# Performance work log

Measured on AMD Instinct MI355X. Metric: run time of the kernel, lower is better.

The kernel has to match this reference:

```python
import jax, jax.numpy as jnp
import numpy as np
import math

EMBED_DIM = 2048
NUM_HEADS = 16
DEPTH = 12
HEAD_DIM = EMBED_DIM // NUM_HEADS // 2  # 64
LAMBDA_INIT = 0.8 - 0.6 * math.exp(-0.3 * DEPTH)


def setup_inputs() -> dict:
    key = jax.random.key(0)
    ks = jax.random.split(key, 9)
    B, T, E = 2, 2048, EMBED_DIM
    s = 1.0 / math.sqrt(E)
    return {
        "query": jax.random.normal(ks[0], (B, T, E), jnp.float32),
        "Wq": jax.random.normal(ks[1], (E, E), jnp.float32) * s,
        "Wk": jax.random.normal(ks[2], (E, E), jnp.float32) * s,
        "Wv": jax.random.normal(ks[3], (E, E), jnp.float32) * s,
        "Wo": jax.random.normal(ks[4], (E, E), jnp.float32) * s,
        "lambda_q1": jax.random.normal(ks[5], (HEAD_DIM,), jnp.float32) * 0.1,
        "lambda_k1": jax.random.normal(ks[6], (HEAD_DIM,), jnp.float32) * 0.1,
        "lambda_q2": jax.random.normal(ks[7], (HEAD_DIM,), jnp.float32) * 0.1,
        "lambda_k2": jax.random.normal(ks[8], (HEAD_DIM,), jnp.float32) * 0.1,
        "subln_weight": jnp.ones((2 * HEAD_DIM,), jnp.float32),
    }


def _diff_attn(query, Wq, Wk, Wv, Wo, lq1, lk1, lq2, lk2, g):
    B, T, E = query.shape
    H, D = NUM_HEADS, HEAD_DIM
    S = T  # self-attention: key = value = query
    scaling = D ** -0.5

    # projections (nn.Linear: x @ W.T)
    q = (query @ Wq.T).reshape(B, T, 2 * H, D).transpose(0, 2, 1, 3)  # [B,2H,T,D]
    k = (query @ Wk.T).reshape(B, S, 2 * H, D).transpose(0, 2, 1, 3)  # [B,2H,S,D]
    v = (query @ Wv.T).reshape(B, S, H, 2 * D).transpose(0, 2, 1, 3)  # [B,H,S,2D]

    q = q * scaling
    attn = jnp.einsum("bhtd,bhsd->bhts", q, k)  # [B,2H,T,S]
    attn = jnp.nan_to_num(attn)
    # default causal mask (offset = S - T = 0)
    causal = jnp.triu(jnp.full((T, S), -jnp.inf, attn.dtype), k=1)
    attn = jax.nn.softmax(attn + causal, axis=-1)

    lam1 = jnp.exp(jnp.sum(lq1 * lk1))
    lam2 = jnp.exp(jnp.sum(lq2 * lk2))
    lam = lam1 - lam2 + LAMBDA_INIT

    attn = attn.reshape(B, H, 2, T, S)
    attn = attn[:, :, 0] - lam * attn[:, :, 1]  # differential combine [B,H,T,S]

    out = jnp.einsum("bhts,bhsd->bhtd", attn, v)  # [B,H,T,2D]
    # RMSNorm over last dim (2D), eps=1e-5, elementwise affine g
    rms = jax.lax.rsqrt(jnp.mean(out * out, axis=-1, keepdims=True) + 1e-5)
    out = out * rms * g
    out = out * (1.0 - LAMBDA_INIT)
    out = out.transpose(0, 2, 1, 3).reshape(B, T, H * 2 * D)
    return out @ Wo.T


def reference(query, Wq, Wk, Wv, Wo, lambda_q1, lambda_k1, lambda_q2, lambda_k2, subln_weight):
    return _diff_attn(query, Wq, Wk, Wv, Wo, lambda_q1, lambda_k1, lambda_q2, lambda_k2, subln_weight)
```

## Files before the change

### kernel.cpp

```cpp
#include <hip/hip_runtime.h>


#define B_SZ   2
#define T_LEN  2048
#define E_DIM  2048
#define M_ROWS 4096
#define NH     16
#define HH     32
#define HD     64
#define VD     128
#define NQT    16
#define QKLD   4096

#define LAMBDA_INIT_F 0.7836057665316239f
#define ONE_MINUS_LI  0.2163942334683761f

typedef __attribute__((ext_vector_type(4))) float          f32x4;
typedef __attribute__((ext_vector_type(8))) short          s16x8;
typedef __attribute__((ext_vector_type(4))) unsigned short u16x4;
typedef __attribute__((ext_vector_type(8))) __bf16         bf16x8;

typedef const __attribute__((address_space(1))) unsigned int* gas_t;
typedef __attribute__((address_space(3))) unsigned int*       las_t;
__device__ __forceinline__ void gl_lds16(const void* g, void* l) {
  __builtin_amdgcn_global_load_lds((gas_t)g, (las_t)l, 16, 0, 0);
}

__device__ __forceinline__ float bf2f(unsigned short h) {
  union { unsigned u; float f; } v; v.u = ((unsigned)h) << 16; return v.f;
}
__device__ __forceinline__ unsigned short f2bf(float f) {
  union { float f; unsigned u; } v; v.f = f;
  return (unsigned short)((v.u + 0x7fffu + ((v.u >> 16) & 1u)) >> 16);
}
__device__ __forceinline__ unsigned fbits(float f) {
  union { float f; unsigned u; } v; v.f = f; return v.u;
}
__device__ __forceinline__ float bits2f(unsigned u) {
  union { unsigned u; float f; } v; v.u = u; return v.f;
}

__global__ __launch_bounds__(256) void cast_bf16(const float* __restrict__ in,
                                                 unsigned short* __restrict__ out,
                                                 int n4, float scale) {
  int i = blockIdx.x * 256 + threadIdx.x;
  const int stride = gridDim.x * 256;
  for (; i < n4; i += stride) {
    f32x4 v = ((const f32x4*)in)[i];
    u16x4 o;
    o[0] = f2bf(v[0] * scale); o[1] = f2bf(v[1] * scale);
    o[2] = f2bf(v[2] * scale); o[3] = f2bf(v[3] * scale);
    ((u16x4*)out)[i] = o;
  }
}

template <int OUT_F32>
__global__ __launch_bounds__(512, 2) void gemm8(const unsigned short* __restrict__ A,
                                                const unsigned short* __restrict__ Bm,
                                                void* __restrict__ Cout,
                                                int M, int N, int K, float alpha,
                                                int gx) {
  __shared__ unsigned short AS[2][2][128 * 64];
  __shared__ unsigned short BS[2][2][128 * 64];
  const int tid = threadIdx.x, lane = tid & 63, wave = tid >> 6;
  const int wm = wave >> 2, wn = wave & 3;
  const int lr = lane & 15, g = lane >> 4;
  const int nwg = gridDim.x;
  const int cpx = nwg >> 3;
  const int bid = blockIdx.x;
  const int swz = (bid & 7) * cpx + (bid >> 3);
  const int bx = swz % gx, by = swz / gx;
  const int m0 = bx * 256, n0 = by * 256;

  f32x4 acc[8][4] = {};
  const int NT = K >> 6;

  auto stageA = [&](int t, int h) {
#pragma unroll
    for (int l = 0; l < 2; ++l) {
      const int ci = l * 512 + tid;
      const int row = ci >> 3;
      const int cs = (ci & 7) ^ (row & 7);
      gl_lds16(A + (size_t)(m0 + h * 128 + row) * K + t * 64 + cs * 8,
               &AS[t & 1][h][(l * 512 + wave * 64) * 8]);
    }
  };
  auto stageB = [&](int t, int h) {
#pragma unroll
    for (int l = 0; l < 2; ++l) {
      const int ci = l * 512 + tid;
      const int row = ci >> 3;
      const int cs = (ci & 7) ^ (row & 7);
      gl_lds16(Bm + (size_t)(n0 + h * 128 + row) * K + t * 64 + cs * 8,
               &BS[t & 1][h][(l * 512 + wave * 64) * 8]);
    }
  };

  stageA(0, 0); stageB(0, 0); stageA(0, 1); stageB(0, 1);
  asm volatile("s_waitcnt vmcnt(4)" ::: "memory");
  __builtin_amdgcn_sched_barrier(0);
  __builtin_amdgcn_s_barrier();

  for (int t = 0; t < NT; ++t) {
    const int cur = t & 1;
    const bool pf = (t + 1 < NT);
#pragma unroll
    for (int p = 0; p < 4; ++p) {
      const int mh = p & 1;
      const int nh = p >> 1;
      bf16x8 af[4][2], bfr[2][2];
#pragma unroll
      for (int mf = 0; mf < 4; ++mf) {
        const int r = wm * 64 + mf * 16 + lr;
#pragma unroll
        for (int kc = 0; kc < 2; ++kc)
          af[mf][kc] = *(const bf16x8*)(&AS[cur][mh][r * 64 + (((kc * 4 + g) ^ (r & 7)) * 8)]);
      }
#pragma unroll
      for (int nf = 0; nf < 2; ++nf) {
        const int r = wn * 32 + nf * 16 + lr;
#pragma unroll
        for (int kc = 0; kc < 2; ++kc)
          bfr[nf][kc] = *(const bf16x8*)(&BS[cur][nh][r * 64 + (((kc * 4 + g) ^ (r & 7)) * 8)]);
      }
      if (pf) {
        if (p == 0)      stageA(t + 1, 0);
        else if (p == 1) stageB(t + 1, 0);
        else if (p == 2) stageA(t + 1, 1);
        else             stageB(t + 1, 1);
      }
      __builtin_amdgcn_s_barrier();
      __builtin_amdgcn_s_setprio(1);
#pragma unroll
      for (int mf = 0; mf < 4; ++mf)
#pragma unroll
        for (int nf = 0; nf < 2; ++nf)
#pragma unroll
          for (int kc = 0; kc < 2; ++kc)
            acc[mh * 4 + mf][nh * 2 + nf] =
                __builtin_amdgcn_mfma_f32_16x16x32_bf16(af[mf][kc], bfr[nf][kc],
                                                        acc[mh * 4 + mf][nh * 2 + nf],
                                                        0, 0, 0);
      __builtin_amdgcn_s_setprio(0);
      if (p == 2) asm volatile("s_waitcnt vmcnt(6)" ::: "memory");
      else        asm volatile("s_waitcnt vmcnt(4)" ::: "memory");
      __builtin_amdgcn_sched_barrier(0);
      __builtin_amdgcn_s_barrier();
    }
  }

#pragma unroll
  for (int mh = 0; mh < 2; ++mh)
#pragma unroll
    for (int mf = 0; mf < 4; ++mf)
#pragma unroll
      for (int nh = 0; nh < 2; ++nh)
#pragma unroll
        for (int nf = 0; nf < 2; ++nf) {
          const int rowb = m0 + mh * 128 + wm * 64 + mf * 16 + g * 4;
          const int col  = n0 + nh * 128 + wn * 32 + nf * 16 + lr;
#pragma unroll
          for (int r = 0; r < 4; ++r) {
            const float v = acc[mh * 4 + mf][nh * 2 + nf][r] * alpha;
            const size_t idx = (size_t)(rowb + r) * N + col;
            if (OUT_F32) ((float*)Cout)[idx] = v;
            else         ((unsigned short*)Cout)[idx] = f2bf(v);
          }
        }
}

__device__ __forceinline__ void stage_kv(const unsigned short* __restrict__ Kbase,
                                         const unsigned short* __restrict__ Vbase,
                                         int s0, unsigned short* KsBuf,
                                         unsigned short* VtBuf, int tid, int wave) {
#pragma unroll
  for (int j = 0; j < 2; ++j) {
    const int ci = tid + j * 256;
    const int s = ci >> 3;
    const int cs = (ci & 7) ^ (s & 7);
    gl_lds16(Kbase + (size_t)(s0 + s) * QKLD + cs * 8, KsBuf + (wave * 64 + j * 256) * 8);
  }
#pragma unroll
  for (int cc = 0; cc < 4; ++cc) {
    const int ci = tid + cc * 256;
    const int d = ci >> 3;
    const int cs = (ci & 7) ^ (d & 7);
    gl_lds16(Vbase + (size_t)d * M_ROWS + s0 + cs * 8, VtBuf + (wave * 64 + cc * 256) * 8);
  }
}

__global__ __launch_bounds__(256, 2) void flash_attn_mfma(
    const unsigned short* __restrict__ QK,
    const unsigned short* __restrict__ VT,
    float* __restrict__ Ohalf) {
  const int pr = blockIdx.x;
  const int hh = blockIdx.y;
  const int b  = blockIdx.z;
  const int tid = threadIdx.x, lane = tid & 63, wave = tid >> 6;
  const int g = lane >> 4, lr = lane & 15;
  const int h = hh >> 1;
  const size_t bT = (size_t)b * T_LEN;

  __shared__ unsigned short Ks[2][64 * 64];
  __shared__ unsigned short Vt[2][128 * 64];
  __shared__ unsigned short Pl[128 * 64];

  const unsigned short* Kbase = QK + bT * QKLD + E_DIM + hh * HD;
  const unsigned short* Vbase = VT + (size_t)(h * VD) * M_ROWS + b * T_LEN;

#pragma unroll 1
  for (int half = 0; half < 2; ++half) {
    const int qt = half ? (NQT - 1 - pr) : pr;
    const int qbase = qt * 128;
    const int rw0 = qbase + wave * 32;

    bf16x8 qf[2][2];
#pragma unroll
    for (int mi = 0; mi < 2; ++mi)
#pragma unroll
      for (int kc = 0; kc < 2; ++kc) {
        const int row = qbase + wave * 32 + mi * 16 + lr;
        qf[mi][kc] = *(const bf16x8*)(QK + (bT + row) * QKLD + hh * HD + kc * 32 + g * 8);
      }

    f32x4 Oa[2][8];
#pragma unroll
    for (int mi = 0; mi < 2; ++mi)
#pragma unroll
      for (int dv = 0; dv < 8; ++dv) Oa[mi][dv] = (f32x4){0.f, 0.f, 0.f, 0.f};
    float m_run[2][4], l_part[2][4];
#pragma unroll
    for (int mi = 0; mi < 2; ++mi)
#pragma unroll
      for (int r = 0; r < 4; ++r) { m_run[mi][r] = -1e30f; l_part[mi][r] = 0.f; }

    const int nsteps = 2 * qt + 2;
    __syncthreads();
    stage_kv(Kbase, Vbase, 0, Ks[0], Vt[0], tid, wave);
    int cb = 0;

    for (int ti = 0; ti < nsteps; ++ti) {
      const int s0 = ti * 64;
      __syncthreads();
      if (ti + 1 < nsteps)
        stage_kv(Kbase, Vbase, s0 + 64, Ks[cb ^ 1], Vt[cb ^ 1], tid, wave);

      if (s0 <= rw0 + 31) {
        const unsigned short* ks = Ks[cb];
        const unsigned short* vt = Vt[cb];
        bf16x8 kb[4][2];
#pragma unroll
        for (int nj = 0; nj < 4; ++nj)
#pragma unroll
          for (int kc = 0; kc < 2; ++kc) {
            const int srow = nj * 16 + lr;
            kb[nj][kc] = *(const bf16x8*)(&ks[srow * 64 + (((kc * 4 + g) ^ (srow & 7)) * 8)]);
          }
        f32x4 Sa[2][4];
#pragma unroll
        for (int mi = 0; mi < 2; ++mi)
#pragma unroll
          for (int nj = 0; nj < 4; ++nj) {
            f32x4 acc = (f32x4){0.f, 0.f, 0.f, 0.f};
#pragma unroll
            for (int kc = 0; kc < 2; ++kc)
              acc = __builtin_amdgcn_mfma_f32_16x16x32_bf16(qf[mi][kc], kb[nj][kc], acc, 0, 0, 0);
            Sa[mi][nj] = acc;
          }

        const bool needmask = (s0 + 63) > rw0;
        float mx[2][4];
        bool anew = false;
#pragma unroll
        for (int mi = 0; mi < 2; ++mi)
#pragma unroll
          for (int r = 0; r < 4; ++r) {
            const int rowq = rw0 + mi * 16 + g * 4 + r;
            float m0v = -1e30f;
#pragma unroll
            for (int nj = 0; nj < 4; ++nj) {
              float v = Sa[mi][nj][r];
              if (needmask && (s0 + nj * 16 + lr > rowq)) v = -1e30f;
              Sa[mi][nj][r] = v;
              m0v = fmaxf(m0v, v);
            }
            m0v = fmaxf(m0v, __shfl_xor(m0v, 1));
            m0v = fmaxf(m0v, __shfl_xor(m0v, 2));
            m0v = fmaxf(m0v, __shfl_xor(m0v, 4));
            m0v = fmaxf(m0v, __shfl_xor(m0v, 8));
            mx[mi][r] = m0v;
            anew |= (m0v > m_run[mi][r] + 8.0f);
          }

        if (__any(anew)) {
#pragma unroll
          for (int mi = 0; mi < 2; ++mi)
#pragma unroll
            for (int r = 0; r < 4; ++r) {
              const float mn = fmaxf(m_run[mi][r], mx[mi][r]);
              const float rs = __expf(m_run[mi][r] - mn);
              m_run[mi][r] = mn;
              l_part[mi][r] *= rs;
#pragma unroll
              for (int dv = 0; dv < 8; ++dv) Oa[mi][dv][r] *= rs;
            }
        }

#pragma unroll
        for (int mi = 0; mi < 2; ++mi) {
#pragma unroll
          for (int r = 0; r < 4; ++r) {
            const int row = wave * 32 + mi * 16 + g * 4 + r;
            float ps = 0.f;
#pragma unroll
            for (int nj = 0; nj < 4; ++nj) {
              const float p = __expf(Sa[mi][nj][r] - m_run[mi][r]);
              const unsigned u = fbits(p);
              const int chunk = (nj * 2 + (lr >> 3)) ^ (row & 7);
              Pl[row * 64 + chunk * 8 + (lr & 7)] = (unsigned short)(u >> 16);
              ps += bits2f(u & 0xffff0000u);
            }
            l_part[mi][r] += ps;
          }
        }

        bf16x8 pa[2][2];
#pragma unroll
        for (int mi = 0; mi < 2; ++mi)
#pragma unroll
          for (int kc = 0; kc < 2; ++kc) {
            const int row = wave * 32 + mi * 16 + lr;
            pa[mi][kc] = *(const bf16x8*)(&Pl[row * 64 + (((kc * 4 + g) ^ (row & 7)) * 8)]);
          }
#pragma unroll
        for (int dv = 0; dv < 8; ++dv) {
          bf16x8 vb[2];
#pragma unroll
          for (int kc = 0; kc < 2; ++kc) {
            const int d = dv * 16 + lr;
            vb[kc] = *(const bf16x8*)(&vt[d * 64 + (((kc * 4 + g) ^ (d & 7)) * 8)]);
          }
#pragma unroll
          for (int mi = 0; mi < 2; ++mi)
#pragma unroll
            for (int kc = 0; kc < 2; ++kc)
              Oa[mi][dv] = __builtin_amdgcn_mfma_f32_16x16x32_bf16(pa[mi][kc], vb[kc],
                                                                   Oa[mi][dv], 0, 0, 0);
        }
      }
      cb ^= 1;
    }

#pragma unroll
    for (int mi = 0; mi < 2; ++mi)
#pragma unroll
      for (int r = 0; r < 4; ++r) {
        float ls = l_part[mi][r];
        ls += __shfl_xor(ls, 1);
        ls += __shfl_xor(ls, 2);
        ls += __shfl_xor(ls, 4);
        ls += __shfl_xor(ls, 8);
        const float rn = 1.f / ls;
        const int t = qbase + wave * 32 + mi * 16 + g * 4 + r;
        float* orow = Ohalf + ((size_t)(b * HH + hh) * T_LEN + t) * VD;
#pragma unroll
        for (int dv = 0; dv < 8; ++dv)
          orow[dv * 16 + lr] = Oa[mi][dv][r] * rn;
      }
  }
}

__global__ __launch_bounds__(256) void combine_norm(
    const float* __restrict__ Oh,
    const float* __restrict__ lq1, const float* __restrict__ lk1,
    const float* __restrict__ lq2, const float* __restrict__ lk2,
    const float* __restrict__ g,
    unsigned short* __restrict__ Act) {
  const int lane = threadIdx.x & 63;
  const int r = blockIdx.x * 4 + (threadIdx.x >> 6);
  const int hd = r & 15;
  const int t = (r >> 4) & 2047;
  const int b = r >> 15;
  float p1 = lq1[lane] * lk1[lane];
  float p2 = lq2[lane] * lk2[lane];
#pragma unroll
  for (int o = 1; o < 64; o <<= 1) { p1 += __shfl_xor(p1, o); p2 += __shfl_xor(p2, o); }
  const float lam = __expf(p1) - __expf(p2) + LAMBDA_INIT_F;
  const float* o0 = Oh + ((size_t)(b * HH + 2 * hd) * T_LEN + t) * VD;
  const float* o1 = o0 + (size_t)T_LEN * VD;
  const float x0 = o0[lane]      - lam * o1[lane];
  const float x1 = o0[lane + 64] - lam * o1[lane + 64];
  float ss = x0 * x0 + x1 * x1;
#pragma unroll
  for (int o = 1; o < 64; o <<= 1) ss += __shfl_xor(ss, o);
  const float s = rsqrtf(ss * (1.f / 128.f) + 1e-5f) * ONE_MINUS_LI;
  unsigned short* arow = Act + ((size_t)(b * T_LEN + t) * E_DIM + hd * VD);
  arow[lane]      = f2bf(x0 * s * g[lane]);
  arow[lane + 64] = f2bf(x1 * s * g[lane + 64]);
}

extern "C" void kernel_launch(void* const* d_in, const int* in_sizes, int n_in,
                              void* d_out, int out_size, void* d_ws, size_t ws_size,
                              hipStream_t stream) {
  (void)in_sizes; (void)n_in; (void)out_size; (void)ws_size;
  const float* x   = (const float*)d_in[0];
  const float* Wq  = (const float*)d_in[1];
  const float* Wk  = (const float*)d_in[2];
  const float* Wv  = (const float*)d_in[3];
  const float* Wo  = (const float*)d_in[4];
  const float* lq1 = (const float*)d_in[5];
  const float* lk1 = (const float*)d_in[6];
  const float* lq2 = (const float*)d_in[7];
  const float* lk2 = (const float*)d_in[8];
  const float* g   = (const float*)d_in[9];

  char* p = (char*)d_ws;
  unsigned short* XBF = (unsigned short*)p; p += (size_t)M_ROWS * E_DIM * 2;
  unsigned short* WQB = (unsigned short*)p; p += (size_t)E_DIM * E_DIM * 2;
  unsigned short* WKB = (unsigned short*)p; p += (size_t)E_DIM * E_DIM * 2;
  unsigned short* WVB = (unsigned short*)p; p += (size_t)E_DIM * E_DIM * 2;
  unsigned short* WOB = (unsigned short*)p; p += (size_t)E_DIM * E_DIM * 2;
  unsigned short* QKB = (unsigned short*)p; p += (size_t)M_ROWS * QKLD * 2;
  unsigned short* VTB = (unsigned short*)p; p += (size_t)M_ROWS * E_DIM * 2;
  float*          OH  = (float*)p;          p += (size_t)B_SZ * HH * T_LEN * VD * 4;
  unsigned short* ACT = (unsigned short*)p; p += (size_t)M_ROWS * E_DIM * 2;

  cast_bf16<<<2048, 256, 0, stream>>>(x,  XBF, M_ROWS * E_DIM / 4, 1.0f);
  cast_bf16<<<1024, 256, 0, stream>>>(Wq, WQB, E_DIM * E_DIM / 4, 0.125f);
  cast_bf16<<<1024, 256, 0, stream>>>(Wk, WKB, E_DIM * E_DIM / 4, 1.0f);
  cast_bf16<<<1024, 256, 0, stream>>>(Wv, WVB, E_DIM * E_DIM / 4, 1.0f);
  cast_bf16<<<1024, 256, 0, stream>>>(Wo, WOB, E_DIM * E_DIM / 4, 1.0f);

  gemm8<0><<<(M_ROWS / 256) * (2 * E_DIM / 256), 512, 0, stream>>>(
      XBF, WQB, QKB, M_ROWS, 2 * E_DIM, E_DIM, 1.0f, M_ROWS / 256);
  gemm8<0><<<(E_DIM / 256) * (M_ROWS / 256), 512, 0, stream>>>(
      WVB, XBF, VTB, E_DIM, M_ROWS, E_DIM, 1.0f, E_DIM / 256);

  flash_attn_mfma<<<dim3(NQT / 2, HH, B_SZ), 256, 0, stream>>>(QKB, VTB, OH);

  combine_norm<<<B_SZ * T_LEN * NH / 4, 256, 0, stream>>>(OH, lq1, lk1, lq2, lk2, g, ACT);

  gemm8<1><<<(M_ROWS / 256) * (E_DIM / 256), 512, 0, stream>>>(
      ACT, WOB, d_out, M_ROWS, E_DIM, E_DIM, 1.0f, M_ROWS / 256);
}
```

Before: 485.0 us.

## Fuse bf16 casts into one launch and use a 128x128 GEMM for V/out projections

Merges the five separate fp32-to-bf16 cast launches into one kernel that indexes the contiguous workspace (x, Wq, Wk, Wv, Wo laid out back to back), cutting launch overhead. It also adds a simpler single-buffered 128x128-tile GEMM with 256 threads and uses it for the V projection and the output projection in place of the double-buffered 256x256 gemm8. This gives more workgroups, but the new GEMM loses the LDS double buffering that overlapped loads with MFMA work, and its 128-row stride assumes the cast buffers are contiguous in the workspace.

```diff
diff --git a/kernel.cpp b/kernel.cpp
--- a/kernel.cpp
+++ b/kernel.cpp
@@ -40,17 +40,29 @@
   union { unsigned u; float f; } v; v.u = u; return v.f;
 }
 
-__global__ __launch_bounds__(256) void cast_bf16(const float* __restrict__ in,
-                                                 unsigned short* __restrict__ out,
-                                                 int n4, float scale) {
+__global__ __launch_bounds__(256) void cast_fused(
+    const float* __restrict__ x,  const float* __restrict__ Wq,
+    const float* __restrict__ Wk, const float* __restrict__ Wv,
+    const float* __restrict__ Wo, unsigned short* __restrict__ dst) {
+  const int X4 = M_ROWS * E_DIM / 4;
+  const int W4 = E_DIM * E_DIM / 4;
+  const int total = X4 + 4 * W4;
   int i = blockIdx.x * 256 + threadIdx.x;
   const int stride = gridDim.x * 256;
-  for (; i < n4; i += stride) {
-    f32x4 v = ((const f32x4*)in)[i];
+  for (; i < total; i += stride) {
+    const float* src; int off; float scale = 1.0f;
+    if (i < X4) { src = x; off = i; }
+    else {
+      const int j = i - X4;
+      const int w = j >> 20; off = j & (W4 - 1);
+      src = (w == 0) ? Wq : (w == 1) ? Wk : (w == 2) ? Wv : Wo;
+      if (w == 0) scale = 0.125f;
+    }
+    f32x4 v = ((const f32x4*)src)[off];
     u16x4 o;
     o[0] = f2bf(v[0] * scale); o[1] = f2bf(v[1] * scale);
     o[2] = f2bf(v[2] * scale); o[3] = f2bf(v[3] * scale);
-    ((u16x4*)out)[i] = o;
+    ((u16x4*)dst)[i] = o;
   }
 }
 
@@ -169,6 +181,72 @@
         }
 }
 
+template <int OUT_F32>
+__global__ __launch_bounds__(256, 3) void gemm_bt(const unsigned short* __restrict__ A,
+                                                  const unsigned short* __restrict__ Bm,
+                                                  void* __restrict__ Cout,
+                                                  int M, int N, int K, float alpha) {
+  __shared__ unsigned short As[128 * 64];
+  __shared__ unsigned short Bs[128 * 64];
+  const int tid  = threadIdx.x;
+  const int lane = tid & 63;
+  const int wave = tid >> 6;
+  const int wr = wave >> 1, wc = wave & 1;
+  const int lrow = lane & 15, lkb = lane >> 4;
+  const int m0 = blockIdx.x * 128, n0 = blockIdx.y * 128;
+
+  f32x4 acc[4][4] = {};
+
+  for (int k0 = 0; k0 < K; k0 += 64) {
+#pragma unroll
+    for (int it = 0; it < 4; ++it) {
+      const int ci  = tid + it * 256;
+      const int row = ci >> 3;
+      const int cs  = (ci & 7) ^ (row & 7);
+      const int rb  = (wave * 64 + it * 256) * 8;
+      gl_lds16(A  + (size_t)(m0 + row) * K + k0 + cs * 8, &As[rb]);
+      gl_lds16(Bm + (size_t)(n0 + row) * K + k0 + cs * 8, &Bs[rb]);
+    }
+    __syncthreads();
+#pragma unroll
+    for (int kc = 0; kc < 2; ++kc) {
+      bf16x8 af[4], bfr[4];
+#pragma unroll
+      for (int mi = 0; mi < 4; ++mi) {
+        const int r = wr * 64 + mi * 16 + lrow;
+        af[mi] = *(const bf16x8*)(&As[r * 64 + (((kc * 4 + lkb) ^ (r & 7)) * 8)]);
+      }
+#pragma unroll
+      for (int ni = 0; ni < 4; ++ni) {
+        const int r = wc * 64 + ni * 16 + lrow;
+        bfr[ni] = *(const bf16x8*)(&Bs[r * 64 + (((kc * 4 + lkb) ^ (r & 7)) * 8)]);
+      }
+#pragma unroll
+      for (int mi = 0; mi < 4; ++mi)
+#pragma unroll
+        for (int ni = 0; ni < 4; ++ni)
+          acc[mi][ni] = __builtin_amdgcn_mfma_f32_16x16x32_bf16(af[mi], bfr[ni],
+                                                                acc[mi][ni], 0, 0, 0);
+    }
+    __syncthreads();
+  }
+#pragma unroll
+  for (int mi = 0; mi < 4; ++mi) {
+#pragma unroll
+    for (int ni = 0; ni < 4; ++ni) {
+      const int mb = m0 + wr * 64 + mi * 16 + lkb * 4;
+      const int nn = n0 + wc * 64 + ni * 16 + lrow;
+#pragma unroll
+      for (int r = 0; r < 4; ++r) {
+        const float v = acc[mi][ni][r] * alpha;
+        const size_t idx = (size_t)(mb + r) * N + nn;
+        if (OUT_F32) ((float*)Cout)[idx] = v;
+        else         ((unsigned short*)Cout)[idx] = f2bf(v);
+      }
+    }
+  }
+}
+
 __device__ __forceinline__ void stage_kv(const unsigned short* __restrict__ Kbase,
                                          const unsigned short* __restrict__ Vbase,
                                          int s0, unsigned short* KsBuf,
@@ -425,21 +503,17 @@
   float*          OH  = (float*)p;          p += (size_t)B_SZ * HH * T_LEN * VD * 4;
   unsigned short* ACT = (unsigned short*)p; p += (size_t)M_ROWS * E_DIM * 2;
 
-  cast_bf16<<<2048, 256, 0, stream>>>(x,  XBF, M_ROWS * E_DIM / 4, 1.0f);
-  cast_bf16<<<1024, 256, 0, stream>>>(Wq, WQB, E_DIM * E_DIM / 4, 0.125f);
-  cast_bf16<<<1024, 256, 0, stream>>>(Wk, WKB, E_DIM * E_DIM / 4, 1.0f);
-  cast_bf16<<<1024, 256, 0, stream>>>(Wv, WVB, E_DIM * E_DIM / 4, 1.0f);
-  cast_bf16<<<1024, 256, 0, stream>>>(Wo, WOB, E_DIM * E_DIM / 4, 1.0f);
+  cast_fused<<<2048, 256, 0, stream>>>(x, Wq, Wk, Wv, Wo, XBF);
 
   gemm8<0><<<(M_ROWS / 256) * (2 * E_DIM / 256), 512, 0, stream>>>(
       XBF, WQB, QKB, M_ROWS, 2 * E_DIM, E_DIM, 1.0f, M_ROWS / 256);
-  gemm8<0><<<(E_DIM / 256) * (M_ROWS / 256), 512, 0, stream>>>(
-      WVB, XBF, VTB, E_DIM, M_ROWS, E_DIM, 1.0f, E_DIM / 256);
+  dim3 gt(E_DIM / 128, M_ROWS / 128);
+  gemm_bt<0><<<gt, 256, 0, stream>>>(WVB, XBF, VTB, E_DIM, M_ROWS, E_DIM, 1.0f);
 
   flash_attn_mfma<<<dim3(NQT / 2, HH, B_SZ), 256, 0, stream>>>(QKB, VTB, OH);
 
   combine_norm<<<B_SZ * T_LEN * NH / 4, 256, 0, stream>>>(OH, lq1, lk1, lq2, lk2, g, ACT);
 
-  gemm8<1><<<(M_ROWS / 256) * (E_DIM / 256), 512, 0, stream>>>(
-      ACT, WOB, d_out, M_ROWS, E_DIM, E_DIM, 1.0f, M_ROWS / 256);
-}
+  dim3 gg(M_ROWS / 128, E_DIM / 128);
+  gemm_bt<1><<<gg, 256, 0, stream>>>(ACT, WOB, d_out, M_ROWS, E_DIM, E_DIM, 1.0f);
+}
```

After: 423.5 us. 12.7% less time.
